# Kernel tuning notes

Measured on AMD Instinct MI355X. Metric: run time of the kernel, lower is better.

## Reference

```python
import jax, jax.numpy as jnp
import numpy as np

N_EMBD = 1024
N_HEADS = 16
HEAD_SIZE = N_EMBD // N_HEADS
BLOCK_SIZE = 2048
BATCH = 2
SEQ = 2048
EPS = 1e-5


def setup_inputs() -> dict:
    key = jax.random.key(0)
    ks = jax.random.split(key, 12)
    s = 0.02
    x = jax.random.normal(ks[0], (BATCH, SEQ, N_EMBD), dtype=jnp.float32)
    # per-head Q/K/V weights concatenated: [n_embd, n_heads*head_size]
    Wq = jax.random.normal(ks[1], (N_EMBD, N_EMBD), dtype=jnp.float32) * s
    Wk = jax.random.normal(ks[2], (N_EMBD, N_EMBD), dtype=jnp.float32) * s
    Wv = jax.random.normal(ks[3], (N_EMBD, N_EMBD), dtype=jnp.float32) * s
    Wproj = jax.random.normal(ks[4], (N_EMBD, N_EMBD), dtype=jnp.float32) * s
    bproj = jnp.zeros((N_EMBD,), dtype=jnp.float32)
    W1 = jax.random.normal(ks[5], (N_EMBD, 4 * N_EMBD), dtype=jnp.float32) * s
    b1 = jnp.zeros((4 * N_EMBD,), dtype=jnp.float32)
    W2 = jax.random.normal(ks[6], (4 * N_EMBD, N_EMBD), dtype=jnp.float32) * s
    b2 = jnp.zeros((N_EMBD,), dtype=jnp.float32)
    ln1_w = jnp.ones((N_EMBD,), dtype=jnp.float32)
    ln1_b = jnp.zeros((N_EMBD,), dtype=jnp.float32)
    ln2_w = jnp.ones((N_EMBD,), dtype=jnp.float32)
    ln2_b = jnp.zeros((N_EMBD,), dtype=jnp.float32)
    return dict(x=x, Wq=Wq, Wk=Wk, Wv=Wv, Wproj=Wproj, bproj=bproj,
                W1=W1, b1=b1, W2=W2, b2=b2,
                ln1_w=ln1_w, ln1_b=ln1_b, ln2_w=ln2_w, ln2_b=ln2_b)


def _layer_norm(x, w, b):
    mu = jnp.mean(x, axis=-1, keepdims=True)
    var = jnp.var(x, axis=-1, keepdims=True)
    return (x - mu) * jax.lax.rsqrt(var + EPS) * w + b


def reference(x, Wq, Wk, Wv, Wproj, bproj, W1, b1, W2, b2, ln1_w, ln1_b, ln2_w, ln2_b):
    B, T, C = x.shape
    # --- attention sub-block (pre-LN) ---
    h = _layer_norm(x, ln1_w, ln1_b)
    # project then split heads: [B,T,H,D] -> [B,H,T,D]
    def split(W):
        return (h @ W).reshape(B, T, N_HEADS, HEAD_SIZE).transpose(0, 2, 1, 3)
    q, k, v = split(Wq), split(Wk), split(Wv)
    # NOTE: original code scales by C**-0.5 with C = n_embd (not head_size)
    scores = jnp.einsum('bhtd,bhsd->bhts', q, k) * (C ** -0.5)  # [B,H,T,T]
    causal = jnp.tril(jnp.ones((T, T), dtype=bool))
    scores = jnp.where(causal, scores, -jnp.inf)
    wei = jax.nn.softmax(scores, axis=-1)
    attn = jnp.einsum('bhts,bhsd->bhtd', wei, v)  # [B,H,T,D]
    attn = attn.transpose(0, 2, 1, 3).reshape(B, T, C)  # concat heads
    x = x + attn @ Wproj + bproj
    # --- FFN sub-block (pre-LN) ---
    h2 = _layer_norm(x, ln2_w, ln2_b)
    ff = jax.nn.relu(h2 @ W1 + b1) @ W2 + b2
    return x + ff
```

## Files before the change

kernel.cpp:

```cpp
#include <hip/hip_runtime.h>
#include <cstdint>

typedef __attribute__((ext_vector_type(8))) __bf16 bf16_8;
typedef __attribute__((ext_vector_type(4))) __bf16 bf16_4;
typedef __attribute__((ext_vector_type(4))) float f32x4;

#define QSCALE 0.045084220027780106f

__device__ __forceinline__ void gld_lds16(const __bf16* g, __bf16* l) {
  __builtin_amdgcn_global_load_lds(
      (const __attribute__((address_space(1))) void*)(void*)g,
      (__attribute__((address_space(3))) void*)l, 16, 0, 0);
}

__global__ __launch_bounds__(256) void convt_k(
    const float* __restrict__ Wq, const float* __restrict__ Wk,
    const float* __restrict__ Wv, const float* __restrict__ Wp,
    const float* __restrict__ W1, const float* __restrict__ W2,
    __bf16* __restrict__ WqT, __bf16* __restrict__ WkT,
    __bf16* __restrict__ WvT, __bf16* __restrict__ WpT,
    __bf16* __restrict__ W1T, __bf16* __restrict__ W2T) {
  int bid = blockIdx.x;
  const float* in; __bf16* outp; int Kd, Nd, tile;
  if (bid < 4096) {
    int m = bid >> 10; tile = bid & 1023; Kd = 1024; Nd = 1024;
    in   = m == 0 ? Wq  : m == 1 ? Wk  : m == 2 ? Wv  : Wp;
    outp = m == 0 ? WqT : m == 1 ? WkT : m == 2 ? WvT : WpT;
  } else if (bid < 8192) {
    tile = bid - 4096; Kd = 1024; Nd = 4096; in = W1; outp = W1T;
  } else {
    tile = bid - 8192; Kd = 4096; Nd = 1024; in = W2; outp = W2T;
  }
  int tilesN = Nd >> 5;
  int tk = tile / tilesN, tn = tile % tilesN;
  int k0 = tk * 32, n0 = tn * 32;
  __shared__ float tbuf[32][33];
  int tx = threadIdx.x & 31, ty = threadIdx.x >> 5;
#pragma unroll
  for (int i = 0; i < 4; ++i)
    tbuf[ty + i * 8][tx] = in[(size_t)(k0 + ty + i * 8) * Nd + (n0 + tx)];
  __syncthreads();
#pragma unroll
  for (int i = 0; i < 4; ++i)
    outp[(size_t)(n0 + ty + i * 8) * Kd + (k0 + tx)] = (__bf16)tbuf[tx][ty + i * 8];
}

__global__ __launch_bounds__(256) void ln_k(const float* __restrict__ x,
                                            const float* __restrict__ w,
                                            const float* __restrict__ b,
                                            __bf16* __restrict__ out) {
  int row = blockIdx.x;
  int tid = threadIdx.x;
  f32x4 v = *(const f32x4*)(x + (size_t)row * 1024 + tid * 4);
  float s = v[0] + v[1] + v[2] + v[3];
  float sq = v[0] * v[0] + v[1] * v[1] + v[2] * v[2] + v[3] * v[3];
#pragma unroll
  for (int m = 1; m < 64; m <<= 1) { s += __shfl_xor(s, m); sq += __shfl_xor(sq, m); }
  __shared__ float rs[4], rq[4];
  int wave = tid >> 6, lane = tid & 63;
  if (lane == 0) { rs[wave] = s; rq[wave] = sq; }
  __syncthreads();
  s  = rs[0] + rs[1] + rs[2] + rs[3];
  sq = rq[0] + rq[1] + rq[2] + rq[3];
  float mu   = s * (1.f / 1024.f);
  float var  = sq * (1.f / 1024.f) - mu * mu;
  float rstd = rsqrtf(var + 1e-5f);
  f32x4 wv = *(const f32x4*)(w + tid * 4);
  f32x4 bv = *(const f32x4*)(b + tid * 4);
  bf16_4 o;
#pragma unroll
  for (int i = 0; i < 4; ++i) o[i] = (__bf16)((v[i] - mu) * rstd * wv[i] + bv[i]);
  *(bf16_4*)(out + (size_t)row * 1024 + tid * 4) = o;
}

template <int MODE, int BM, int BN, int BK>
__global__ __launch_bounds__(256) void gemm_k(
    const __bf16* __restrict__ A,
    const __bf16* __restrict__ B0, const __bf16* __restrict__ B1,
    const __bf16* __restrict__ B2,
    __bf16* __restrict__ O0, __bf16* __restrict__ O1, __bf16* __restrict__ O2,
    float* __restrict__ Of,
    const float* __restrict__ bias, const float* __restrict__ res,
    int K, int Nchunk, int nBlkM, int nBlkN) {
  constexpr int NC = BK / 8;
  constexpr int MT = BM / 32, NT = BN / 32;
  constexpr int KK = BK / 32;
  constexpr int RPC = 64 / NC;
  constexpr int CA = BM / RPC / 4;
  constexpr int CB = BN / RPC / 4;
  __shared__ __align__(16) __bf16 As[2][BM * BK];
  __shared__ __align__(16) __bf16 Bs[2][BN * BK];
  int chunk = blockIdx.y;
  const __bf16* Bt = chunk == 0 ? B0 : (chunk == 1 ? B1 : B2);
  __bf16* Ob       = chunk == 0 ? O0 : (chunk == 1 ? O1 : O2);
  int pid = blockIdx.x;
  const int GM = 8;
  int perG = GM * nBlkN;
  int gid = pid / perG;
  int fm = gid * GM;
  int gsz = min(nBlkM - fm, GM);
  int bm = fm + (pid % gsz);
  int bn = (pid % perG) / gsz;
  int m0 = bm * BM, n0 = bn * BN;
  int tid = threadIdx.x, wave = tid >> 6, lane = tid & 63;
  int quad = lane >> 4, l16 = lane & 15;
  int wm = (wave & 1) * (BM / 2), wn = (wave >> 1) * (BN / 2);
  int srow = lane / NC, schunk = lane % NC;

  f32x4 z = {0.f, 0.f, 0.f, 0.f};
  f32x4 acc[MT][NT];
#pragma unroll
  for (int mt = 0; mt < MT; ++mt)
#pragma unroll
    for (int nt = 0; nt < NT; ++nt) acc[mt][nt] = z;

  const __bf16* Ag = A  + (size_t)m0 * K;
  const __bf16* Bg = Bt + (size_t)n0 * K;

  auto stage = [&](int k0, int buf) {
#pragma unroll
    for (int i = 0; i < CA; ++i) {
      int r0 = (wave * CA + i) * RPC;
      int gc = schunk ^ ((r0 + srow) & (NC - 1));
      gld_lds16(Ag + (size_t)(r0 + srow) * K + k0 + gc * 8, &As[buf][r0 * BK]);
    }
#pragma unroll
    for (int i = 0; i < CB; ++i) {
      int r0 = (wave * CB + i) * RPC;
      int gc = schunk ^ ((r0 + srow) & (NC - 1));
      gld_lds16(Bg + (size_t)(r0 + srow) * K + k0 + gc * 8, &Bs[buf][r0 * BK]);
    }
  };

  auto compute = [&](int buf) {
#pragma unroll
    for (int kk = 0; kk < KK; ++kk) {
      bf16_8 af[MT], bfr[NT];
#pragma unroll
      for (int t = 0; t < MT; ++t) {
        int r = wm + t * 16 + l16;
        int lc = (kk * 4 + quad) ^ (r & (NC - 1));
        af[t] = *(const bf16_8*)(&As[buf][r * BK + lc * 8]);
      }
#pragma unroll
      for (int t = 0; t < NT; ++t) {
        int r = wn + t * 16 + l16;
        int lc = (kk * 4 + quad) ^ (r & (NC - 1));
        bfr[t] = *(const bf16_8*)(&Bs[buf][r * BK + lc * 8]);
      }
#pragma unroll
      for (int mt = 0; mt < MT; ++mt)
#pragma unroll
        for (int nt = 0; nt < NT; ++nt)
          acc[mt][nt] = __builtin_amdgcn_mfma_f32_16x16x32_bf16(af[mt], bfr[nt],
                                                                acc[mt][nt], 0, 0, 0);
    }
  };

  int niter = K / BK;
  stage(0, 0);
  __syncthreads();
  for (int it = 0; it < niter - 1; ++it) {
    stage((it + 1) * BK, (it + 1) & 1);
    compute(it & 1);
    __syncthreads();
  }
  compute((niter - 1) & 1);

  if (MODE == 0 && chunk == 2) {
#pragma unroll
    for (int mt = 0; mt < MT; ++mt) {
      int mbase = m0 + wm + mt * 16 + quad * 4;
      int bb = mbase >> 11, tt = mbase & 2047;
#pragma unroll
      for (int nt = 0; nt < NT; ++nt) {
        int n = n0 + wn + nt * 16 + l16;
        bf16_4 pk;
#pragma unroll
        for (int r = 0; r < 4; ++r) pk[r] = (__bf16)acc[mt][nt][r];
        *(bf16_4*)(O2 + ((size_t)((bb * 16 + (n >> 6)) * 64 + (n & 63))) * 2048 + tt) = pk;
      }
    }
    return;
  }

  float oscale = (MODE == 0 && chunk == 0) ? QSCALE : 1.0f;
#pragma unroll
  for (int mt = 0; mt < MT; ++mt) {
#pragma unroll
    for (int r = 0; r < 4; ++r) {
      int m = m0 + wm + mt * 16 + quad * 4 + r;
      size_t rowo = (size_t)m * Nchunk;
#pragma unroll
      for (int nt = 0; nt < NT; ++nt) {
        int n = n0 + wn + nt * 16 + l16;
        float v = acc[mt][nt][r];
        if (MODE == 0) {
          Ob[rowo + n] = (__bf16)(v * oscale);
        } else if (MODE == 1) {
          v += bias[n]; v = v > 0.f ? v : 0.f;
          Ob[rowo + n] = (__bf16)v;
        } else {
          v += bias[n] + res[rowo + n];
          Of[rowo + n] = v;
        }
      }
    }
  }
}

__global__ __launch_bounds__(256, 3) void attn_k(const __bf16* __restrict__ Q,
                                                 const __bf16* __restrict__ K,
                                                 const __bf16* __restrict__ Vt,
                                                 __bf16* __restrict__ O) {
  __shared__ __align__(16) __bf16 Pls[4][32 * 72];
  __shared__ __align__(16) __bf16 Xbuf[2][32 * 72];
  __shared__ float Lbuf[4][32][4];

  int i = blockIdx.x;
  int bh = i & 31, j = i >> 5;
  int h = bh & 15, b = bh >> 4;
  int tid = threadIdx.x, wave = tid >> 6, lane = tid & 63;
  int quad = lane >> 4, l16 = lane & 15;
  int qg_lo = j, qg_hi = 63 - j;
  int t_lo = (j >> 1) + 1;
  int u0 = wave == 0 ? 0 : wave == 1 ? 9 : wave == 2 ? 17 : 25;
  int u1 = wave == 0 ? 9 : wave == 1 ? 17 : wave == 2 ? 25 : 33;
  int lo0 = u0, lo1 = min(u1, t_lo);
  int hi0 = max(u0, t_lo) - t_lo, hi1 = u1 - t_lo;

  const __bf16* Kb = K + (size_t)(b * 2048) * 1024 + h * 64;
  const __bf16* Vh = Vt + (size_t)((b * 16 + h) * 64) * 2048;
  __bf16* Pw = &Pls[wave][0];

  f32x4 z = {0.f, 0.f, 0.f, 0.f};
  bf16_8 qf[2][2], kfr[4][2], vfr[4][2];
  f32x4 ot[2][4];
  float l_acc[2];

  auto loadK = [&](int kt) {
#pragma unroll
    for (int kk = 0; kk < 4; ++kk) {
      const __bf16* kr = Kb + (size_t)(kt + kk * 16 + l16) * 1024 + quad * 8;
      kfr[kk][0] = *(const bf16_8*)(kr);
      kfr[kk][1] = *(const bf16_8*)(kr + 32);
    }
  };
  auto loadV = [&](int kt) {
#pragma unroll
    for (int dt = 0; dt < 4; ++dt) {
      const __bf16* vr = Vh + (size_t)(dt * 16 + l16) * 2048 + kt + quad * 8;
      vfr[dt][0] = *(const bf16_8*)(vr);
      vfr[dt][1] = *(const bf16_8*)(vr + 32);
    }
  };

  auto run = [&](int qg, int it0, int it1) {
#pragma unroll
    for (int g = 0; g < 2; ++g) {
      const __bf16* Qg = Q + ((size_t)(b * 2048 + qg * 32 + g * 16 + l16)) * 1024 + h * 64;
      qf[g][0] = *(const bf16_8*)(Qg + quad * 8);
      qf[g][1] = *(const bf16_8*)(Qg + 32 + quad * 8);
    }
#pragma unroll
    for (int g = 0; g < 2; ++g) {
#pragma unroll
      for (int dt = 0; dt < 4; ++dt) ot[g][dt] = z;
      l_acc[g] = 0.f;
    }
    if (it0 >= it1) return;
    int qw = qg * 32;
    loadK(it0 * 64);
    for (int it = it0; it < it1; ++it) {
      int kt = it * 64;
      bool masked = (kt + 63 > qw);
      f32x4 sf[2][4];
#pragma unroll
      for (int kk = 0; kk < 4; ++kk) {
#pragma unroll
        for (int g = 0; g < 2; ++g) {
          f32x4 a = z;
          a = __builtin_amdgcn_mfma_f32_16x16x32_bf16(kfr[kk][0], qf[g][0], a, 0, 0, 0);
          a = __builtin_amdgcn_mfma_f32_16x16x32_bf16(kfr[kk][1], qf[g][1], a, 0, 0, 0);
          sf[g][kk] = a;
        }
      }
      if (it + 1 < it1) loadK((it + 1) * 64);
      loadV(kt);
#pragma unroll
      for (int g = 0; g < 2; ++g) {
        int qrow = qw + g * 16 + l16;
#pragma unroll
        for (int kk = 0; kk < 4; ++kk) {
          bf16_4 pk;
#pragma unroll
          for (int r = 0; r < 4; ++r) {
            float x = sf[g][kk][r];
            if (masked && (kt + kk * 16 + quad * 4 + r > qrow)) x = -1e30f;
            float pp = __builtin_amdgcn_exp2f(x);
            l_acc[g] += pp;
            pk[r] = (__bf16)pp;
          }
          *(bf16_4*)(Pw + (g * 16 + l16) * 72 + kk * 16 + quad * 4) = pk;
        }
      }
      bf16_8 pf[2][2];
#pragma unroll
      for (int g = 0; g < 2; ++g) {
        pf[g][0] = *(const bf16_8*)(Pw + (g * 16 + l16) * 72 + quad * 8);
        pf[g][1] = *(const bf16_8*)(Pw + (g * 16 + l16) * 72 + 32 + quad * 8);
      }
#pragma unroll
      for (int dt = 0; dt < 4; ++dt) {
#pragma unroll
        for (int g = 0; g < 2; ++g) {
          ot[g][dt] = __builtin_amdgcn_mfma_f32_16x16x32_bf16(vfr[dt][0], pf[g][0], ot[g][dt], 0, 0, 0);
          ot[g][dt] = __builtin_amdgcn_mfma_f32_16x16x32_bf16(vfr[dt][1], pf[g][1], ot[g][dt], 0, 0, 0);
        }
      }
    }
  };

  auto putP = [&](__bf16* Ob, float (*Lb)[4]) {
#pragma unroll
    for (int g = 0; g < 2; ++g) {
#pragma unroll
      for (int dt = 0; dt < 4; ++dt) {
        bf16_4 pk;
#pragma unroll
        for (int r = 0; r < 4; ++r) pk[r] = (__bf16)ot[g][dt][r];
        *(bf16_4*)(Ob + (g * 16 + l16) * 72 + dt * 16 + quad * 4) = pk;
      }
      Lb[g * 16 + l16][quad] = l_acc[g];
    }
  };
  auto addP = [&](const __bf16* Ob, const float (*Lb)[4]) {
#pragma unroll
    for (int g = 0; g < 2; ++g) {
#pragma unroll
      for (int dt = 0; dt < 4; ++dt) {
        bf16_4 pk = *(const bf16_4*)(Ob + (g * 16 + l16) * 72 + dt * 16 + quad * 4);
#pragma unroll
        for (int r = 0; r < 4; ++r) ot[g][dt][r] += (float)pk[r];
      }
      l_acc[g] += Lb[g * 16 + l16][quad];
    }
  };
  auto writeO = [&](int qg) {
#pragma unroll
    for (int g = 0; g < 2; ++g) {
      float l = l_acc[g];
      l += __shfl_xor(l, 16);
      l += __shfl_xor(l, 32);
      float inv = 1.0f / l;
      size_t base = (size_t)(b * 2048 + qg * 32 + g * 16 + l16) * 1024 + h * 64;
#pragma unroll
      for (int dt = 0; dt < 4; ++dt) {
        bf16_4 ok;
#pragma unroll
        for (int r = 0; r < 4; ++r) ok[r] = (__bf16)(ot[g][dt][r] * inv);
        *(bf16_4*)(O + base + dt * 16 + quad * 4) = ok;
      }
    }
  };

  if (wave == 0) {
    run(qg_hi, hi0, hi1);
    putP(&Xbuf[0][0], Lbuf[0]);
    run(qg_lo, lo0, lo1);
    __syncthreads();
    addP(&Xbuf[1][0], Lbuf[1]);
    writeO(qg_lo);
  } else if (wave == 1) {
    run(qg_lo, lo0, lo1);
    putP(&Xbuf[1][0], Lbuf[1]);
    run(qg_hi, hi0, hi1);
    putP(&Pls[1][0], Lbuf[2]);
    __syncthreads();
  } else if (wave == 2) {
    run(qg_hi, hi0, hi1);
    putP(&Pls[2][0], Lbuf[3]);
    __syncthreads();
  } else {
    run(qg_hi, hi0, hi1);
    __syncthreads();
    addP(&Pls[1][0], Lbuf[2]);
    addP(&Pls[2][0], Lbuf[3]);
    addP(&Xbuf[0][0], Lbuf[0]);
    writeO(qg_hi);
  }
}

extern "C" void kernel_launch(void* const* d_in, const int* in_sizes, int n_in,
                              void* d_out, int out_size, void* d_ws,
                              size_t ws_size, hipStream_t stream) {
  const float* x   = (const float*)d_in[0];
  const float* Wq  = (const float*)d_in[1];
  const float* Wk  = (const float*)d_in[2];
  const float* Wv  = (const float*)d_in[3];
  const float* Wp  = (const float*)d_in[4];
  const float* bp  = (const float*)d_in[5];
  const float* W1  = (const float*)d_in[6];
  const float* b1  = (const float*)d_in[7];
  const float* W2  = (const float*)d_in[8];
  const float* b2  = (const float*)d_in[9];
  const float* l1w = (const float*)d_in[10];
  const float* l1b = (const float*)d_in[11];
  const float* l2w = (const float*)d_in[12];
  const float* l2b = (const float*)d_in[13];
  float* out = (float*)d_out;
  char* ws = (char*)d_ws;
  const size_t MB = 1024ull * 1024ull;
  __bf16* WqT = (__bf16*)(ws + 0 * MB);
  __bf16* WkT = (__bf16*)(ws + 2 * MB);
  __bf16* WvT = (__bf16*)(ws + 4 * MB);
  __bf16* WpT = (__bf16*)(ws + 6 * MB);
  __bf16* W1T = (__bf16*)(ws + 8 * MB);
  __bf16* W2T = (__bf16*)(ws + 16 * MB);
  __bf16* hb  = (__bf16*)(ws + 24 * MB);
  __bf16* Qb  = (__bf16*)(ws + 32 * MB);
  __bf16* Kb_ = (__bf16*)(ws + 40 * MB);
  __bf16* Vt  = (__bf16*)(ws + 48 * MB);
  __bf16* Ab  = (__bf16*)(ws + 56 * MB);
  __bf16* F1  = (__bf16*)(ws + 64 * MB);

  convt_k<<<12288, 256, 0, stream>>>(Wq, Wk, Wv, Wp, W1, W2,
                                     WqT, WkT, WvT, WpT, W1T, W2T);
  ln_k<<<4096, 256, 0, stream>>>(x, l1w, l1b, hb);
  gemm_k<0, 128, 128, 32><<<dim3(256, 3), 256, 0, stream>>>(
      hb, WqT, WkT, WvT, Qb, Kb_, Vt, nullptr, nullptr, nullptr,
      1024, 1024, 32, 8);
  attn_k<<<1024, 256, 0, stream>>>(Qb, Kb_, Vt, Ab);
  gemm_k<2, 64, 64, 64><<<dim3(1024, 1), 256, 0, stream>>>(
      Ab, WpT, WpT, WpT, nullptr, nullptr, nullptr, out, bp, x,
      1024, 1024, 64, 16);
  ln_k<<<4096, 256, 0, stream>>>(out, l2w, l2b, hb);
  gemm_k<1, 128, 128, 32><<<dim3(1024, 1), 256, 0, stream>>>(
      hb, W1T, W1T, W1T, F1, F1, F1, nullptr, b1, nullptr,
      1024, 4096, 32, 32);
  gemm_k<2, 64, 64, 64><<<dim3(1024, 1), 256, 0, stream>>>(
      F1, W2T, W2T, W2T, nullptr, nullptr, nullptr, out, b2, out,
      4096, 1024, 64, 16);
}
```

Baseline: 378.2 us.

## Share K/V register buffer and raise attention occupancy to four blocks per CU

The attention kernel now reuses one register array for K and V fragments, computes softmax per K sub-tile right after its QK MFMAs instead of holding all scores live, and reorders the PV MFMAs by half. The goal is to cut register pressure enough to raise launch bounds from 3 to 4 blocks per CU for more latency hiding. In exchange the next K tile is loaded only after the PV MFMAs, so K prefetch no longer overlaps the softmax and PV work, which may expose more global load latency.

```diff
diff --git a/kernel.cpp b/kernel.cpp
--- a/kernel.cpp
+++ b/kernel.cpp
@@ -209,7 +209,7 @@
   }
 }
 
-__global__ __launch_bounds__(256, 3) void attn_k(const __bf16* __restrict__ Q,
+__global__ __launch_bounds__(256, 4) void attn_k(const __bf16* __restrict__ Q,
                                                  const __bf16* __restrict__ K,
                                                  const __bf16* __restrict__ Vt,
                                                  __bf16* __restrict__ O) {
@@ -234,7 +234,7 @@
   __bf16* Pw = &Pls[wave][0];
 
   f32x4 z = {0.f, 0.f, 0.f, 0.f};
-  bf16_8 qf[2][2], kfr[4][2], vfr[4][2];
+  bf16_8 qf[2][2], kv[4][2];
   f32x4 ot[2][4];
   float l_acc[2];
 
@@ -242,16 +242,16 @@
 #pragma unroll
     for (int kk = 0; kk < 4; ++kk) {
       const __bf16* kr = Kb + (size_t)(kt + kk * 16 + l16) * 1024 + quad * 8;
-      kfr[kk][0] = *(const bf16_8*)(kr);
-      kfr[kk][1] = *(const bf16_8*)(kr + 32);
+      kv[kk][0] = *(const bf16_8*)(kr);
+      kv[kk][1] = *(const bf16_8*)(kr + 32);
     }
   };
   auto loadV = [&](int kt) {
 #pragma unroll
     for (int dt = 0; dt < 4; ++dt) {
       const __bf16* vr = Vh + (size_t)(dt * 16 + l16) * 2048 + kt + quad * 8;
-      vfr[dt][0] = *(const bf16_8*)(vr);
-      vfr[dt][1] = *(const bf16_8*)(vr + 32);
+      kv[dt][0] = *(const bf16_8*)(vr);
+      kv[dt][1] = *(const bf16_8*)(vr + 32);
     }
   };
 
@@ -274,28 +274,23 @@
     for (int it = it0; it < it1; ++it) {
       int kt = it * 64;
       bool masked = (kt + 63 > qw);
-      f32x4 sf[2][4];
 #pragma unroll
       for (int kk = 0; kk < 4; ++kk) {
+        f32x4 s[2];
 #pragma unroll
         for (int g = 0; g < 2; ++g) {
           f32x4 a = z;
-          a = __builtin_amdgcn_mfma_f32_16x16x32_bf16(kfr[kk][0], qf[g][0], a, 0, 0, 0);
-          a = __builtin_amdgcn_mfma_f32_16x16x32_bf16(kfr[kk][1], qf[g][1], a, 0, 0, 0);
-          sf[g][kk] = a;
+          a = __builtin_amdgcn_mfma_f32_16x16x32_bf16(kv[kk][0], qf[g][0], a, 0, 0, 0);
+          a = __builtin_amdgcn_mfma_f32_16x16x32_bf16(kv[kk][1], qf[g][1], a, 0, 0, 0);
+          s[g] = a;
         }
-      }
-      if (it + 1 < it1) loadK((it + 1) * 64);
-      loadV(kt);
-#pragma unroll
-      for (int g = 0; g < 2; ++g) {
-        int qrow = qw + g * 16 + l16;
-#pragma unroll
-        for (int kk = 0; kk < 4; ++kk) {
+#pragma unroll
+        for (int g = 0; g < 2; ++g) {
+          int qrow = qw + g * 16 + l16;
           bf16_4 pk;
 #pragma unroll
           for (int r = 0; r < 4; ++r) {
-            float x = sf[g][kk][r];
+            float x = s[g][r];
             if (masked && (kt + kk * 16 + quad * 4 + r > qrow)) x = -1e30f;
             float pp = __builtin_amdgcn_exp2f(x);
             l_acc[g] += pp;
@@ -304,20 +299,18 @@
           *(bf16_4*)(Pw + (g * 16 + l16) * 72 + kk * 16 + quad * 4) = pk;
         }
       }
-      bf16_8 pf[2][2];
-#pragma unroll
-      for (int g = 0; g < 2; ++g) {
-        pf[g][0] = *(const bf16_8*)(Pw + (g * 16 + l16) * 72 + quad * 8);
-        pf[g][1] = *(const bf16_8*)(Pw + (g * 16 + l16) * 72 + 32 + quad * 8);
-      }
-#pragma unroll
-      for (int dt = 0; dt < 4; ++dt) {
-#pragma unroll
-        for (int g = 0; g < 2; ++g) {
-          ot[g][dt] = __builtin_amdgcn_mfma_f32_16x16x32_bf16(vfr[dt][0], pf[g][0], ot[g][dt], 0, 0, 0);
-          ot[g][dt] = __builtin_amdgcn_mfma_f32_16x16x32_bf16(vfr[dt][1], pf[g][1], ot[g][dt], 0, 0, 0);
+      loadV(kt);
+#pragma unroll
+      for (int hf = 0; hf < 2; ++hf) {
+        bf16_8 pf0 = *(const bf16_8*)(Pw + (l16) * 72 + hf * 32 + quad * 8);
+        bf16_8 pf1 = *(const bf16_8*)(Pw + (16 + l16) * 72 + hf * 32 + quad * 8);
+#pragma unroll
+        for (int dt = 0; dt < 4; ++dt) {
+          ot[0][dt] = __builtin_amdgcn_mfma_f32_16x16x32_bf16(kv[dt][hf], pf0, ot[0][dt], 0, 0, 0);
+          ot[1][dt] = __builtin_amdgcn_mfma_f32_16x16x32_bf16(kv[dt][hf], pf1, ot[1][dt], 0, 0, 0);
         }
       }
+      if (it + 1 < it1) loadK((it + 1) * 64);
     }
   };
 
```

Result: faster. 346.5 us (-8.4%).
